# Performance work log

Measured on AMD Instinct MI355X. Metric: run time of the kernel, lower is better.

## Reference

```python
import jax, jax.numpy as jnp
import numpy as np

P = 2  # pooling_size

def setup_inputs() -> dict:
    key = jax.random.key(0)
    k1, k2, k3 = jax.random.split(key, 3)
    B, n, D = 16, 4096, 1024
    x = jax.random.normal(k1, (B, n, D), dtype=jnp.float32)
    W1 = jax.random.normal(k2, (D, D), dtype=jnp.float32) * (1.0 / np.sqrt(D))
    b1 = jnp.zeros((D,), dtype=jnp.float32)
    W2 = jax.random.normal(k3, (D, 1), dtype=jnp.float32) * (1.0 / np.sqrt(D))
    b2 = jnp.zeros((1,), dtype=jnp.float32)
    return {"x": x, "W1": W1, "b1": b1, "W2": W2, "b2": b2}

def reference(x, W1, b1, W2, b2):
    # x: [B, n, D] with n a perfect square; pool 2x2 windows via attention.
    B, n, D = x.shape
    s = int(n ** 0.5)
    g = s // P  # grid of regions per side
    # [B, g, P, g, P, D] -> [B, g, g, P, P, D] -> [B, R, P*P, D]
    # region order matches the original double loop (row-major over i, j).
    xg = (x.reshape(B, g, P, g, P, D)
            .transpose(0, 1, 3, 2, 4, 5)
            .reshape(B, g * g, P * P, D))
    # MLP scores (dropout is identity in eval mode)
    h = jax.nn.relu(jnp.einsum('brkd,de->brke', xg, W1) + b1)
    logits = jnp.einsum('brkd,d->brk', h, W2[:, 0]) + b2[0]
    alpha = jax.nn.softmax(logits, axis=-1)  # softmax over the P*P window
    # weighted sum over window -> [B, R, D]
    return jnp.einsum('brk,brkd->brd', alpha, xg)
```

## Files before the change

kernel.cpp:

```cpp
#include <hip/hip_runtime.h>
#include <hip/hip_bf16.h>

typedef float f32x4 __attribute__((ext_vector_type(4)));
typedef __bf16 bf16x8 __attribute__((ext_vector_type(8)));
typedef unsigned short ushort_t;
typedef ushort_t u16x8 __attribute__((ext_vector_type(8)));

#define GLDS16(gp, lp)                                                        \
  __builtin_amdgcn_global_load_lds(                                           \
      (__attribute__((address_space(1))) void*)(gp),                          \
      (__attribute__((address_space(3))) void*)(lp), 16, 0, 0)

__device__ __forceinline__ ushort_t f2bf(float f) {
  unsigned u = __float_as_uint(f);
  unsigned r = u + 0x7fffu + ((u >> 16) & 1u);
  return (ushort_t)(r >> 16);
}

__device__ __forceinline__ int swz(int row) {
  return (row & 3) ^ ((row >> 2) & 3);
}

__global__ __launch_bounds__(256) void prep_w1(const float* __restrict__ w1,
                                               ushort_t* __restrict__ w1t) {
  __shared__ ushort_t tile[64][80];
  const int k0 = blockIdx.x * 64;
  const int n0 = blockIdx.y * 64;
  const int tid = threadIdx.x;
#pragma unroll
  for (int it = 0; it < 16; ++it) {
    int idx = it * 256 + tid;
    int k = idx >> 6, n = idx & 63;
    tile[n][k] = f2bf(w1[(size_t)(k0 + k) * 1024 + n0 + n]);
  }
  __syncthreads();
#pragma unroll
  for (int it = 0; it < 2; ++it) {
    int idx = it * 256 + tid;
    int n = idx >> 3, kk = (idx & 7) * 8;
    bf16x8 v = *(const bf16x8*)&tile[n][kk];
    *(bf16x8*)&w1t[(size_t)(n0 + n) * 1024 + k0 + kk] = v;
  }
}

__global__ __launch_bounds__(256) void prep_x(const float* __restrict__ x,
                                              ushort_t* __restrict__ xbf) {
  size_t i = ((size_t)blockIdx.x * 256 + threadIdx.x) * 8;
  float4 a = *(const float4*)(x + i);
  float4 b = *(const float4*)(x + i + 4);
  u16x8 o;
  o[0] = f2bf(a.x); o[1] = f2bf(a.y); o[2] = f2bf(a.z); o[3] = f2bf(a.w);
  o[4] = f2bf(b.x); o[5] = f2bf(b.y); o[6] = f2bf(b.z); o[7] = f2bf(b.w);
  *(u16x8*)(xbf + i) = o;
}

#define FOLD_EPILOGUE(ACC)                                                    \
  {                                                                           \
    float bv[4], wv[4];                                                       \
    _Pragma("unroll") for (int ni = 0; ni < 4; ++ni) {                        \
      int col = nt * 256 + wn + ni * 16 + lc;                                 \
      bv[ni] = b1[col];                                                       \
      wv[ni] = w2[col];                                                       \
    }                                                                         \
    _Pragma("unroll") for (int mi = 0; mi < 4; ++mi)                          \
        _Pragma("unroll") for (int r = 0; r < 4; ++r) {                       \
      float s = 0.f;                                                          \
      _Pragma("unroll") for (int ni = 0; ni < 4; ++ni) {                      \
        float h = ACC[mi][ni][r] + bv[ni];                                    \
        h = h > 0.f ? h : 0.f;                                                \
        s += h * wv[ni];                                                      \
      }                                                                       \
      racc[mi][r] += s;                                                       \
    }                                                                         \
  }

template <bool A_BF16>
__global__ __launch_bounds__(512, 4) void gemm_fused(
    const void* __restrict__ aglob, const ushort_t* __restrict__ w1t,
    const float* __restrict__ b1, const float* __restrict__ w2,
    const float* __restrict__ x, float* __restrict__ out) {
  __shared__ ushort_t As[2][128 * 32];
  __shared__ ushort_t Bs[2][256 * 32];
  __shared__ float lbuf[128];
  __shared__ float abuf[128];

  const int tid = threadIdx.x;
  const int wave = tid >> 6, lane = tid & 63;
  const int quad = lane >> 4, lc = lane & 15;
  const int m0 = blockIdx.x * 128;
  const int wm = (wave & 1) * 64, wn = (wave >> 1) * 64;

  const int rA = tid >> 2, cA = (tid & 3) ^ swz(tid >> 2);
  const int rB0 = tid >> 2, cB0 = (tid & 3) ^ swz(rB0);
  const int rB1 = 128 + (tid >> 2), cB1 = (tid & 3) ^ swz(rB1);

  const ushort_t* abf = nullptr;
  const float* af = nullptr;
  if constexpr (A_BF16) {
    abf = (const ushort_t*)aglob + (size_t)(m0 + rA) * 1024 + cA * 8;
  } else {
    af = (const float*)aglob + (size_t)(m0 + rA) * 1024 + cA * 8;
  }
  const ushort_t* bp0 = w1t + (size_t)rB0 * 1024 + cB0 * 8;
  const ushort_t* bp1 = w1t + (size_t)rB1 * 1024 + cB1 * 8;

  int aoff[4], boff[4];
#pragma unroll
  for (int mi = 0; mi < 4; ++mi) {
    int r = wm + mi * 16 + lc;
    aoff[mi] = r * 32 + (quad ^ swz(r)) * 8;
  }
#pragma unroll
  for (int ni = 0; ni < 4; ++ni) {
    int r = wn + ni * 16 + lc;
    boff[ni] = r * 32 + (quad ^ swz(r)) * 8;
  }

  auto stage = [&](int buf, int nt_, int kt_) {
    const size_t cb = (size_t)nt_ * (256 * 1024);
    const int k0 = kt_ * 32;
    GLDS16(bp0 + cb + k0, &Bs[buf][tid * 8]);
    GLDS16(bp1 + cb + k0, &Bs[buf][(512 + tid) * 8]);
    if constexpr (A_BF16) {
      GLDS16(abf + k0, &As[buf][tid * 8]);
    } else {
      float4 v0 = *(const float4*)(af + k0);
      float4 v1 = *(const float4*)(af + k0 + 4);
      u16x8 o0;
      o0[0] = f2bf(v0.x); o0[1] = f2bf(v0.y); o0[2] = f2bf(v0.z); o0[3] = f2bf(v0.w);
      o0[4] = f2bf(v1.x); o0[5] = f2bf(v1.y); o0[6] = f2bf(v1.z); o0[7] = f2bf(v1.w);
      *(u16x8*)&As[buf][tid * 8] = o0;
    }
  };

  float racc[4][4] = {};

  stage(0, 0, 0);
  __syncthreads();

  for (int nt = 0; nt < 4; ++nt) {
    f32x4 acc[4][4] = {};
#pragma unroll 2
    for (int kt = 0; kt < 32; ++kt) {
      const int cur = kt & 1;
      if (!(nt == 3 && kt == 31)) {
        int nk = kt + 1, nn = nt;
        if (nk == 32) { nk = 0; nn = nt + 1; }
        stage(cur ^ 1, nn, nk);
      }

      bf16x8 afr[4], bfr[4];
#pragma unroll
      for (int mi = 0; mi < 4; ++mi) afr[mi] = *(const bf16x8*)&As[cur][aoff[mi]];
#pragma unroll
      for (int ni = 0; ni < 4; ++ni) bfr[ni] = *(const bf16x8*)&Bs[cur][boff[ni]];
#pragma unroll
      for (int mi = 0; mi < 4; ++mi)
#pragma unroll
        for (int ni = 0; ni < 4; ++ni)
          acc[mi][ni] = __builtin_amdgcn_mfma_f32_16x16x32_bf16(
              afr[mi], bfr[ni], acc[mi][ni], 0, 0, 0);
      __syncthreads();
    }
    FOLD_EPILOGUE(acc)
  }

#pragma unroll
  for (int mi = 0; mi < 4; ++mi)
#pragma unroll
    for (int r = 0; r < 4; ++r)
#pragma unroll
      for (int off = 1; off < 16; off <<= 1)
        racc[mi][r] += __shfl_xor(racc[mi][r], off, 64);
  __syncthreads();
  if (tid < 128) lbuf[tid] = 0.f;
  __syncthreads();
  if (lc == 0) {
#pragma unroll
    for (int mi = 0; mi < 4; ++mi)
#pragma unroll
      for (int r = 0; r < 4; ++r)
        atomicAdd(&lbuf[wm + mi * 16 + quad * 4 + r], racc[mi][r]);
  }
  __syncthreads();

  if (tid < 32) {
    const int j = tid;
    float l0 = lbuf[2 * j], l1 = lbuf[2 * j + 1];
    float l2 = lbuf[64 + 2 * j], l3 = lbuf[65 + 2 * j];
    float mx = fmaxf(fmaxf(l0, l1), fmaxf(l2, l3));
    float e0 = __expf(l0 - mx), e1 = __expf(l1 - mx);
    float e2 = __expf(l2 - mx), e3 = __expf(l3 - mx);
    float inv = 1.0f / (e0 + e1 + e2 + e3);
    abuf[j * 4 + 0] = e0 * inv;
    abuf[j * 4 + 1] = e1 * inv;
    abuf[j * 4 + 2] = e2 * inv;
    abuf[j * 4 + 3] = e3 * inv;
  }
  __syncthreads();

  const int b = blockIdx.x >> 5, ii = blockIdx.x & 31;
  const int jj = tid >> 8, t = tid & 255;
  const float* xs = x + (size_t)m0 * 1024;
  float* orow = out + ((size_t)(b * 1024 + ii * 32)) * 1024;
  for (int j0 = 0; j0 < 32; j0 += 2) {
    int j = j0 + jj;
    float a0 = abuf[j * 4 + 0], a1 = abuf[j * 4 + 1];
    float a2 = abuf[j * 4 + 2], a3 = abuf[j * 4 + 3];
    const float4* p0 = (const float4*)(xs + (size_t)(2 * j) * 1024);
    const float4* p1 = (const float4*)(xs + (size_t)(2 * j + 1) * 1024);
    const float4* p2 = (const float4*)(xs + (size_t)(64 + 2 * j) * 1024);
    const float4* p3 = (const float4*)(xs + (size_t)(65 + 2 * j) * 1024);
    float4 v0 = p0[t], v1 = p1[t], v2 = p2[t], v3 = p3[t];
    float4 o;
    o.x = a0 * v0.x + a1 * v1.x + a2 * v2.x + a3 * v3.x;
    o.y = a0 * v0.y + a1 * v1.y + a2 * v2.y + a3 * v3.y;
    o.z = a0 * v0.z + a1 * v1.z + a2 * v2.z + a3 * v3.z;
    o.w = a0 * v0.w + a1 * v1.w + a2 * v2.w + a3 * v3.w;
    ((float4*)(orow + (size_t)j * 1024))[t] = o;
  }
}

extern "C" void kernel_launch(void* const* d_in, const int* in_sizes, int n_in,
                              void* d_out, int out_size, void* d_ws,
                              size_t ws_size, hipStream_t stream) {
  const float* x  = (const float*)d_in[0];
  const float* W1 = (const float*)d_in[1];
  const float* b1 = (const float*)d_in[2];
  const float* W2 = (const float*)d_in[3];
  float* out = (float*)d_out;

  const size_t XBF_BYTES = 134217728ull;
  const size_t W1T_BYTES = 2097152ull;

  if (ws_size >= XBF_BYTES + W1T_BYTES) {
    ushort_t* xbf = (ushort_t*)d_ws;
    ushort_t* w1t = (ushort_t*)((char*)d_ws + XBF_BYTES);
    prep_x<<<32768, 256, 0, stream>>>(x, xbf);
    prep_w1<<<dim3(16, 16), 256, 0, stream>>>(W1, w1t);
    gemm_fused<true><<<512, 512, 0, stream>>>(xbf, w1t, b1, W2, x, out);
  } else {
    ushort_t* w1t = (ushort_t*)d_ws;
    prep_w1<<<dim3(16, 16), 256, 0, stream>>>(W1, w1t);
    gemm_fused<false><<<512, 512, 0, stream>>>(x, w1t, b1, W2, x, out);
  }
}
```

Measured before the change: 581.2 us.

## Enlarge GEMM tile to 256 rows with triple-buffered LDS pipeline

Doubles the per-block M tile from 128 to 256 rows, so each block reuses every W1 tile across twice as many rows and the grid halves to 256 blocks. The K loop becomes a flattened 128-step loop over a 3-stage LDS ring with raw s_barrier and explicit vmcnt waits, split into two MFMA halves with setprio so loads for step T+2 overlap compute. The cost is higher register and LDS use per block, lower occupancy (launch bounds 2), and only 256 blocks to cover the CUs, plus hand-written waitcnt logic that could be fragile.

```diff
diff --git a/kernel.cpp b/kernel.cpp
--- a/kernel.cpp
+++ b/kernel.cpp
@@ -10,6 +10,9 @@
   __builtin_amdgcn_global_load_lds(                                           \
       (__attribute__((address_space(1))) void*)(gp),                          \
       (__attribute__((address_space(3))) void*)(lp), 16, 0, 0)
+
+#define RAW_BARRIER() asm volatile("s_barrier" ::: "memory")
+#define WAIT_VMCNT(n) asm volatile("s_waitcnt vmcnt(" #n ")" ::: "memory")
 
 __device__ __forceinline__ ushort_t f2bf(float f) {
   unsigned u = __float_as_uint(f);
@@ -62,7 +65,7 @@
       bv[ni] = b1[col];                                                       \
       wv[ni] = w2[col];                                                       \
     }                                                                         \
-    _Pragma("unroll") for (int mi = 0; mi < 4; ++mi)                          \
+    _Pragma("unroll") for (int mi = 0; mi < 8; ++mi)                          \
         _Pragma("unroll") for (int r = 0; r < 4; ++r) {                       \
       float s = 0.f;                                                          \
       _Pragma("unroll") for (int ni = 0; ni < 4; ++ni) {                      \
@@ -75,38 +78,38 @@
   }
 
 template <bool A_BF16>
-__global__ __launch_bounds__(512, 4) void gemm_fused(
+__global__ __launch_bounds__(512, 2) void gemm_fused(
     const void* __restrict__ aglob, const ushort_t* __restrict__ w1t,
     const float* __restrict__ b1, const float* __restrict__ w2,
     const float* __restrict__ x, float* __restrict__ out) {
-  __shared__ ushort_t As[2][128 * 32];
-  __shared__ ushort_t Bs[2][256 * 32];
-  __shared__ float lbuf[128];
-  __shared__ float abuf[128];
+  __shared__ ushort_t As[3][256 * 32];
+  __shared__ ushort_t Bs[3][256 * 32];
+  __shared__ float lbuf[256];
+  __shared__ float abuf[256];
 
   const int tid = threadIdx.x;
   const int wave = tid >> 6, lane = tid & 63;
   const int quad = lane >> 4, lc = lane & 15;
-  const int m0 = blockIdx.x * 128;
-  const int wm = (wave & 1) * 64, wn = (wave >> 1) * 64;
+  const int m0 = blockIdx.x * 256;
+  const int wm = (wave & 1) * 128, wn = (wave >> 1) * 64;
 
   const int rA = tid >> 2, cA = (tid & 3) ^ swz(tid >> 2);
-  const int rB0 = tid >> 2, cB0 = (tid & 3) ^ swz(rB0);
-  const int rB1 = 128 + (tid >> 2), cB1 = (tid & 3) ^ swz(rB1);
-
-  const ushort_t* abf = nullptr;
-  const float* af = nullptr;
+
+  const ushort_t* abf0 = nullptr; const ushort_t* abf1 = nullptr;
+  const float* af0 = nullptr; const float* af1 = nullptr;
   if constexpr (A_BF16) {
-    abf = (const ushort_t*)aglob + (size_t)(m0 + rA) * 1024 + cA * 8;
+    abf0 = (const ushort_t*)aglob + (size_t)(m0 + rA) * 1024 + cA * 8;
+    abf1 = (const ushort_t*)aglob + (size_t)(m0 + 128 + rA) * 1024 + cA * 8;
   } else {
-    af = (const float*)aglob + (size_t)(m0 + rA) * 1024 + cA * 8;
-  }
-  const ushort_t* bp0 = w1t + (size_t)rB0 * 1024 + cB0 * 8;
-  const ushort_t* bp1 = w1t + (size_t)rB1 * 1024 + cB1 * 8;
-
-  int aoff[4], boff[4];
-#pragma unroll
-  for (int mi = 0; mi < 4; ++mi) {
+    af0 = (const float*)aglob + (size_t)(m0 + rA) * 1024 + cA * 8;
+    af1 = (const float*)aglob + (size_t)(m0 + 128 + rA) * 1024 + cA * 8;
+  }
+  const ushort_t* bq0 = w1t + (size_t)rA * 1024 + cA * 8;
+  const ushort_t* bq1 = w1t + (size_t)(128 + rA) * 1024 + cA * 8;
+
+  int aoff[8], boff[4];
+#pragma unroll
+  for (int mi = 0; mi < 8; ++mi) {
     int r = wm + mi * 16 + lc;
     aoff[mi] = r * 32 + (quad ^ swz(r)) * 8;
   }
@@ -116,108 +119,153 @@
     boff[ni] = r * 32 + (quad ^ swz(r)) * 8;
   }
 
-  auto stage = [&](int buf, int nt_, int kt_) {
-    const size_t cb = (size_t)nt_ * (256 * 1024);
-    const int k0 = kt_ * 32;
-    GLDS16(bp0 + cb + k0, &Bs[buf][tid * 8]);
-    GLDS16(bp1 + cb + k0, &Bs[buf][(512 + tid) * 8]);
+  auto stageA = [&](int buf, int T) {
+    const int k0 = (T & 31) * 32;
     if constexpr (A_BF16) {
-      GLDS16(abf + k0, &As[buf][tid * 8]);
+      GLDS16(abf0 + k0, &As[buf][tid * 8]);
+      GLDS16(abf1 + k0, &As[buf][(512 + tid) * 8]);
     } else {
-      float4 v0 = *(const float4*)(af + k0);
-      float4 v1 = *(const float4*)(af + k0 + 4);
-      u16x8 o0;
+      float4 v0 = *(const float4*)(af0 + k0);
+      float4 v1 = *(const float4*)(af0 + k0 + 4);
+      float4 v2 = *(const float4*)(af1 + k0);
+      float4 v3 = *(const float4*)(af1 + k0 + 4);
+      u16x8 o0, o1;
       o0[0] = f2bf(v0.x); o0[1] = f2bf(v0.y); o0[2] = f2bf(v0.z); o0[3] = f2bf(v0.w);
       o0[4] = f2bf(v1.x); o0[5] = f2bf(v1.y); o0[6] = f2bf(v1.z); o0[7] = f2bf(v1.w);
+      o1[0] = f2bf(v2.x); o1[1] = f2bf(v2.y); o1[2] = f2bf(v2.z); o1[3] = f2bf(v2.w);
+      o1[4] = f2bf(v3.x); o1[5] = f2bf(v3.y); o1[6] = f2bf(v3.z); o1[7] = f2bf(v3.w);
       *(u16x8*)&As[buf][tid * 8] = o0;
+      *(u16x8*)&As[buf][(512 + tid) * 8] = o1;
     }
   };
-
-  float racc[4][4] = {};
-
-  stage(0, 0, 0);
-  __syncthreads();
-
-  for (int nt = 0; nt < 4; ++nt) {
-    f32x4 acc[4][4] = {};
-#pragma unroll 2
-    for (int kt = 0; kt < 32; ++kt) {
-      const int cur = kt & 1;
-      if (!(nt == 3 && kt == 31)) {
-        int nk = kt + 1, nn = nt;
-        if (nk == 32) { nk = 0; nn = nt + 1; }
-        stage(cur ^ 1, nn, nk);
-      }
-
-      bf16x8 afr[4], bfr[4];
-#pragma unroll
-      for (int mi = 0; mi < 4; ++mi) afr[mi] = *(const bf16x8*)&As[cur][aoff[mi]];
-#pragma unroll
-      for (int ni = 0; ni < 4; ++ni) bfr[ni] = *(const bf16x8*)&Bs[cur][boff[ni]];
-#pragma unroll
-      for (int mi = 0; mi < 4; ++mi)
-#pragma unroll
-        for (int ni = 0; ni < 4; ++ni)
-          acc[mi][ni] = __builtin_amdgcn_mfma_f32_16x16x32_bf16(
-              afr[mi], bfr[ni], acc[mi][ni], 0, 0, 0);
-      __syncthreads();
+  auto stageB = [&](int buf, int T) {
+    const int k0 = (T & 31) * 32;
+    const size_t cb = (size_t)(T >> 5) * (256 * 1024);
+    GLDS16(bq0 + cb + k0, &Bs[buf][tid * 8]);
+    GLDS16(bq1 + cb + k0, &Bs[buf][(512 + tid) * 8]);
+  };
+
+  float racc[8][4] = {};
+  f32x4 acc[8][4] = {};
+
+  stageA(0, 0); stageB(0, 0);
+  stageA(1, 1); stageB(1, 1);
+  if constexpr (A_BF16) { WAIT_VMCNT(4); } else { WAIT_VMCNT(2);
+    asm volatile("s_waitcnt lgkmcnt(0)" ::: "memory"); }
+  RAW_BARRIER();
+
+  int cur = 0;
+#pragma unroll 1
+  for (int T = 0; T < 128; ++T) {
+    const int nt = T >> 5;
+    int stg = cur + 2; if (stg >= 3) stg -= 3;
+    const bool doStage = (T + 2 < 128);
+
+    if (doStage) stageA(stg, T + 2);
+    bf16x8 afr[4], bfr[4];
+#pragma unroll
+    for (int mi = 0; mi < 4; ++mi) afr[mi] = *(const bf16x8*)&As[cur][aoff[mi]];
+#pragma unroll
+    for (int ni = 0; ni < 4; ++ni) bfr[ni] = *(const bf16x8*)&Bs[cur][boff[ni]];
+    RAW_BARRIER();
+    __builtin_amdgcn_sched_barrier(0);
+    __builtin_amdgcn_s_setprio(1);
+#pragma unroll
+    for (int mi = 0; mi < 4; ++mi)
+#pragma unroll
+      for (int ni = 0; ni < 4; ++ni)
+        acc[mi][ni] = __builtin_amdgcn_mfma_f32_16x16x32_bf16(
+            afr[mi], bfr[ni], acc[mi][ni], 0, 0, 0);
+    __builtin_amdgcn_s_setprio(0);
+    RAW_BARRIER();
+
+    if (doStage) stageB(stg, T + 2);
+    bf16x8 afr2[4];
+#pragma unroll
+    for (int mi = 0; mi < 4; ++mi)
+      afr2[mi] = *(const bf16x8*)&As[cur][aoff[4 + mi]];
+    RAW_BARRIER();
+    __builtin_amdgcn_sched_barrier(0);
+    __builtin_amdgcn_s_setprio(1);
+#pragma unroll
+    for (int mi = 0; mi < 4; ++mi)
+#pragma unroll
+      for (int ni = 0; ni < 4; ++ni)
+        acc[4 + mi][ni] = __builtin_amdgcn_mfma_f32_16x16x32_bf16(
+            afr2[mi], bfr[ni], acc[4 + mi][ni], 0, 0, 0);
+    __builtin_amdgcn_s_setprio(0);
+
+    if constexpr (!A_BF16) asm volatile("s_waitcnt lgkmcnt(0)" ::: "memory");
+    if (T <= 125) { WAIT_VMCNT(4); } else { WAIT_VMCNT(0); }
+    RAW_BARRIER();
+    cur = cur + 1; if (cur >= 3) cur = 0;
+
+    if ((T & 31) == 31) {
+      FOLD_EPILOGUE(acc)
+#pragma unroll
+      for (int mi = 0; mi < 8; ++mi)
+#pragma unroll
+        for (int ni = 0; ni < 4; ++ni) acc[mi][ni] = (f32x4){0.f, 0.f, 0.f, 0.f};
     }
-    FOLD_EPILOGUE(acc)
-  }
-
-#pragma unroll
-  for (int mi = 0; mi < 4; ++mi)
+  }
+
+#pragma unroll
+  for (int mi = 0; mi < 8; ++mi)
 #pragma unroll
     for (int r = 0; r < 4; ++r)
 #pragma unroll
       for (int off = 1; off < 16; off <<= 1)
         racc[mi][r] += __shfl_xor(racc[mi][r], off, 64);
   __syncthreads();
-  if (tid < 128) lbuf[tid] = 0.f;
+  if (tid < 256) lbuf[tid] = 0.f;
   __syncthreads();
   if (lc == 0) {
 #pragma unroll
-    for (int mi = 0; mi < 4; ++mi)
+    for (int mi = 0; mi < 8; ++mi)
 #pragma unroll
       for (int r = 0; r < 4; ++r)
         atomicAdd(&lbuf[wm + mi * 16 + quad * 4 + r], racc[mi][r]);
   }
   __syncthreads();
 
-  if (tid < 32) {
-    const int j = tid;
-    float l0 = lbuf[2 * j], l1 = lbuf[2 * j + 1];
-    float l2 = lbuf[64 + 2 * j], l3 = lbuf[65 + 2 * j];
+  if (tid < 64) {
+    const int s = tid >> 5, j = tid & 31, base = s * 128;
+    float l0 = lbuf[base + 2 * j], l1 = lbuf[base + 2 * j + 1];
+    float l2 = lbuf[base + 64 + 2 * j], l3 = lbuf[base + 65 + 2 * j];
     float mx = fmaxf(fmaxf(l0, l1), fmaxf(l2, l3));
     float e0 = __expf(l0 - mx), e1 = __expf(l1 - mx);
     float e2 = __expf(l2 - mx), e3 = __expf(l3 - mx);
     float inv = 1.0f / (e0 + e1 + e2 + e3);
-    abuf[j * 4 + 0] = e0 * inv;
-    abuf[j * 4 + 1] = e1 * inv;
-    abuf[j * 4 + 2] = e2 * inv;
-    abuf[j * 4 + 3] = e3 * inv;
-  }
-  __syncthreads();
-
-  const int b = blockIdx.x >> 5, ii = blockIdx.x & 31;
+    abuf[tid * 4 + 0] = e0 * inv;
+    abuf[tid * 4 + 1] = e1 * inv;
+    abuf[tid * 4 + 2] = e2 * inv;
+    abuf[tid * 4 + 3] = e3 * inv;
+  }
+  __syncthreads();
+
   const int jj = tid >> 8, t = tid & 255;
-  const float* xs = x + (size_t)m0 * 1024;
-  float* orow = out + ((size_t)(b * 1024 + ii * 32)) * 1024;
-  for (int j0 = 0; j0 < 32; j0 += 2) {
-    int j = j0 + jj;
-    float a0 = abuf[j * 4 + 0], a1 = abuf[j * 4 + 1];
-    float a2 = abuf[j * 4 + 2], a3 = abuf[j * 4 + 3];
-    const float4* p0 = (const float4*)(xs + (size_t)(2 * j) * 1024);
-    const float4* p1 = (const float4*)(xs + (size_t)(2 * j + 1) * 1024);
-    const float4* p2 = (const float4*)(xs + (size_t)(64 + 2 * j) * 1024);
-    const float4* p3 = (const float4*)(xs + (size_t)(65 + 2 * j) * 1024);
-    float4 v0 = p0[t], v1 = p1[t], v2 = p2[t], v3 = p3[t];
-    float4 o;
-    o.x = a0 * v0.x + a1 * v1.x + a2 * v2.x + a3 * v3.x;
-    o.y = a0 * v0.y + a1 * v1.y + a2 * v2.y + a3 * v3.y;
-    o.z = a0 * v0.z + a1 * v1.z + a2 * v2.z + a3 * v3.z;
-    o.w = a0 * v0.w + a1 * v1.w + a2 * v2.w + a3 * v3.w;
-    ((float4*)(orow + (size_t)j * 1024))[t] = o;
+#pragma unroll 1
+  for (int s = 0; s < 2; ++s) {
+    const int g = blockIdx.x * 2 + s;
+    const int b = g >> 5, ii = g & 31;
+    const float* xs = x + (size_t)(m0 + s * 128) * 1024;
+    float* orow = out + ((size_t)(b * 1024 + ii * 32)) * 1024;
+    for (int j0 = 0; j0 < 32; j0 += 2) {
+      int j = j0 + jj;
+      float a0 = abuf[s * 128 + j * 4 + 0], a1 = abuf[s * 128 + j * 4 + 1];
+      float a2 = abuf[s * 128 + j * 4 + 2], a3 = abuf[s * 128 + j * 4 + 3];
+      const float4* p0 = (const float4*)(xs + (size_t)(2 * j) * 1024);
+      const float4* p1 = (const float4*)(xs + (size_t)(2 * j + 1) * 1024);
+      const float4* p2 = (const float4*)(xs + (size_t)(64 + 2 * j) * 1024);
+      const float4* p3 = (const float4*)(xs + (size_t)(65 + 2 * j) * 1024);
+      float4 v0 = p0[t], v1 = p1[t], v2 = p2[t], v3 = p3[t];
+      float4 o;
+      o.x = a0 * v0.x + a1 * v1.x + a2 * v2.x + a3 * v3.x;
+      o.y = a0 * v0.y + a1 * v1.y + a2 * v2.y + a3 * v3.y;
+      o.z = a0 * v0.z + a1 * v1.z + a2 * v2.z + a3 * v3.z;
+      o.w = a0 * v0.w + a1 * v1.w + a2 * v2.w + a3 * v3.w;
+      ((float4*)(orow + (size_t)j * 1024))[t] = o;
+    }
   }
 }
 
@@ -238,10 +286,10 @@
     ushort_t* w1t = (ushort_t*)((char*)d_ws + XBF_BYTES);
     prep_x<<<32768, 256, 0, stream>>>(x, xbf);
     prep_w1<<<dim3(16, 16), 256, 0, stream>>>(W1, w1t);
-    gemm_fused<true><<<512, 512, 0, stream>>>(xbf, w1t, b1, W2, x, out);
+    gemm_fused<true><<<256, 512, 0, stream>>>(xbf, w1t, b1, W2, x, out);
   } else {
     ushort_t* w1t = (ushort_t*)d_ws;
     prep_w1<<<dim3(16, 16), 256, 0, stream>>>(W1, w1t);
-    gemm_fused<false><<<512, 512, 0, stream>>>(x, w1t, b1, W2, x, out);
-  }
-}
+    gemm_fused<false><<<256, 512, 0, stream>>>(x, w1t, b1, W2, x, out);
+  }
+}
```

New measurement: 609.2 us. 1.05x slower.

## Triple-buffer GEMM LDS staging with vmcnt waits and grid-stride prep_x

Applied to the files above, without the earlier changes.

The fused GEMM moves from a double-buffered K loop with a full __syncthreads each step to a flattened 128-step loop over a three-slot LDS ring. Each step prefetches two stages ahead and uses explicit s_waitcnt vmcnt plus a raw s_barrier, so global-to-LDS loads overlap more compute and each barrier waits only for the oldest stage. The bf16 conversion kernel becomes grid-stride with 2048 blocks instead of 32768. The extra LDS buffer may lower occupancy, and the hand-written waitcnt counts must match the loads actually issued or results will be wrong.

```diff
diff --git a/kernel.cpp b/kernel.cpp
--- a/kernel.cpp
+++ b/kernel.cpp
@@ -10,6 +10,9 @@
   __builtin_amdgcn_global_load_lds(                                           \
       (__attribute__((address_space(1))) void*)(gp),                          \
       (__attribute__((address_space(3))) void*)(lp), 16, 0, 0)
+
+#define RAW_BARRIER() asm volatile("s_barrier" ::: "memory")
+#define WAIT_VMCNT(n) asm volatile("s_waitcnt vmcnt(" #n ")" ::: "memory")
 
 __device__ __forceinline__ ushort_t f2bf(float f) {
   unsigned u = __float_as_uint(f);
@@ -45,13 +48,18 @@
 
 __global__ __launch_bounds__(256) void prep_x(const float* __restrict__ x,
                                               ushort_t* __restrict__ xbf) {
-  size_t i = ((size_t)blockIdx.x * 256 + threadIdx.x) * 8;
-  float4 a = *(const float4*)(x + i);
-  float4 b = *(const float4*)(x + i + 4);
-  u16x8 o;
-  o[0] = f2bf(a.x); o[1] = f2bf(a.y); o[2] = f2bf(a.z); o[3] = f2bf(a.w);
-  o[4] = f2bf(b.x); o[5] = f2bf(b.y); o[6] = f2bf(b.z); o[7] = f2bf(b.w);
-  *(u16x8*)(xbf + i) = o;
+  const size_t nchunks = 8388608ull;
+  const size_t stride = (size_t)gridDim.x * 256;
+  for (size_t c = (size_t)blockIdx.x * 256 + threadIdx.x; c < nchunks;
+       c += stride) {
+    size_t i = c * 8;
+    float4 a = *(const float4*)(x + i);
+    float4 b = *(const float4*)(x + i + 4);
+    u16x8 o;
+    o[0] = f2bf(a.x); o[1] = f2bf(a.y); o[2] = f2bf(a.z); o[3] = f2bf(a.w);
+    o[4] = f2bf(b.x); o[5] = f2bf(b.y); o[6] = f2bf(b.z); o[7] = f2bf(b.w);
+    *(u16x8*)(xbf + i) = o;
+  }
 }
 
 #define FOLD_EPILOGUE(ACC)                                                    \
@@ -79,8 +87,8 @@
     const void* __restrict__ aglob, const ushort_t* __restrict__ w1t,
     const float* __restrict__ b1, const float* __restrict__ w2,
     const float* __restrict__ x, float* __restrict__ out) {
-  __shared__ ushort_t As[2][128 * 32];
-  __shared__ ushort_t Bs[2][256 * 32];
+  __shared__ ushort_t As[3 * 128 * 32];
+  __shared__ ushort_t Bs[3 * 256 * 32];
   __shared__ float lbuf[128];
   __shared__ float abuf[128];
 
@@ -116,53 +124,72 @@
     boff[ni] = r * 32 + (quad ^ swz(r)) * 8;
   }
 
-  auto stage = [&](int buf, int nt_, int kt_) {
+  auto stage = [&](int buf, int T_) {
+    const int nt_ = T_ >> 5, kt_ = T_ & 31;
     const size_t cb = (size_t)nt_ * (256 * 1024);
     const int k0 = kt_ * 32;
-    GLDS16(bp0 + cb + k0, &Bs[buf][tid * 8]);
-    GLDS16(bp1 + cb + k0, &Bs[buf][(512 + tid) * 8]);
+    ushort_t* Bsb = Bs + buf * 8192;
+    ushort_t* Asb = As + buf * 4096;
+    GLDS16(bp0 + cb + k0, Bsb + tid * 8);
+    GLDS16(bp1 + cb + k0, Bsb + (512 + tid) * 8);
     if constexpr (A_BF16) {
-      GLDS16(abf + k0, &As[buf][tid * 8]);
+      GLDS16(abf + k0, Asb + tid * 8);
     } else {
       float4 v0 = *(const float4*)(af + k0);
       float4 v1 = *(const float4*)(af + k0 + 4);
-      u16x8 o0;
-      o0[0] = f2bf(v0.x); o0[1] = f2bf(v0.y); o0[2] = f2bf(v0.z); o0[3] = f2bf(v0.w);
-      o0[4] = f2bf(v1.x); o0[5] = f2bf(v1.y); o0[6] = f2bf(v1.z); o0[7] = f2bf(v1.w);
-      *(u16x8*)&As[buf][tid * 8] = o0;
+      u16x8 o;
+      o[0] = f2bf(v0.x); o[1] = f2bf(v0.y); o[2] = f2bf(v0.z); o[3] = f2bf(v0.w);
+      o[4] = f2bf(v1.x); o[5] = f2bf(v1.y); o[6] = f2bf(v1.z); o[7] = f2bf(v1.w);
+      *(u16x8*)(Asb + tid * 8) = o;
     }
   };
 
   float racc[4][4] = {};
-
-  stage(0, 0, 0);
-  __syncthreads();
-
-  for (int nt = 0; nt < 4; ++nt) {
-    f32x4 acc[4][4] = {};
-#pragma unroll 2
-    for (int kt = 0; kt < 32; ++kt) {
-      const int cur = kt & 1;
-      if (!(nt == 3 && kt == 31)) {
-        int nk = kt + 1, nn = nt;
-        if (nk == 32) { nk = 0; nn = nt + 1; }
-        stage(cur ^ 1, nn, nk);
-      }
-
-      bf16x8 afr[4], bfr[4];
-#pragma unroll
-      for (int mi = 0; mi < 4; ++mi) afr[mi] = *(const bf16x8*)&As[cur][aoff[mi]];
-#pragma unroll
-      for (int ni = 0; ni < 4; ++ni) bfr[ni] = *(const bf16x8*)&Bs[cur][boff[ni]];
+  f32x4 acc[4][4] = {};
+
+  stage(0, 0);
+  stage(1, 1);
+  if constexpr (A_BF16) { WAIT_VMCNT(3); }
+  else { WAIT_VMCNT(2); asm volatile("s_waitcnt lgkmcnt(0)" ::: "memory"); }
+  RAW_BARRIER();
+
+  int bc = 0;
+#pragma unroll 1
+  for (int T = 0; T < 128; ++T) {
+    const int nt = T >> 5;
+    int sb = bc + 2; if (sb >= 3) sb -= 3;
+    if (T < 126) stage(sb, T + 2);
+
+    const ushort_t* Asc = As + bc * 4096;
+    const ushort_t* Bsc = Bs + bc * 8192;
+    bf16x8 afr[4], bfr[4];
+#pragma unroll
+    for (int mi = 0; mi < 4; ++mi) afr[mi] = *(const bf16x8*)&Asc[aoff[mi]];
+#pragma unroll
+    for (int ni = 0; ni < 4; ++ni) bfr[ni] = *(const bf16x8*)&Bsc[boff[ni]];
+#pragma unroll
+    for (int mi = 0; mi < 4; ++mi)
+#pragma unroll
+      for (int ni = 0; ni < 4; ++ni)
+        acc[mi][ni] = __builtin_amdgcn_mfma_f32_16x16x32_bf16(
+            afr[mi], bfr[ni], acc[mi][ni], 0, 0, 0);
+
+    if ((T & 31) == 31) {
+      FOLD_EPILOGUE(acc)
 #pragma unroll
       for (int mi = 0; mi < 4; ++mi)
 #pragma unroll
-        for (int ni = 0; ni < 4; ++ni)
-          acc[mi][ni] = __builtin_amdgcn_mfma_f32_16x16x32_bf16(
-              afr[mi], bfr[ni], acc[mi][ni], 0, 0, 0);
-      __syncthreads();
+        for (int ni = 0; ni < 4; ++ni) acc[mi][ni] = (f32x4){0.f, 0.f, 0.f, 0.f};
     }
-    FOLD_EPILOGUE(acc)
+
+    if constexpr (A_BF16) {
+      if (T < 126) { WAIT_VMCNT(3); }
+      else if (T == 126) { WAIT_VMCNT(0); }
+    } else {
+      asm volatile("s_waitcnt vmcnt(0) lgkmcnt(0)" ::: "memory");
+    }
+    if (T < 127) RAW_BARRIER();
+    bc = (bc == 2) ? 0 : bc + 1;
   }
 
 #pragma unroll
@@ -236,7 +263,7 @@
   if (ws_size >= XBF_BYTES + W1T_BYTES) {
     ushort_t* xbf = (ushort_t*)d_ws;
     ushort_t* w1t = (ushort_t*)((char*)d_ws + XBF_BYTES);
-    prep_x<<<32768, 256, 0, stream>>>(x, xbf);
+    prep_x<<<2048, 256, 0, stream>>>(x, xbf);
     prep_w1<<<dim3(16, 16), 256, 0, stream>>>(W1, w1t);
     gemm_fused<true><<<512, 512, 0, stream>>>(xbf, w1t, b1, W2, x, out);
   } else {
```

New measurement: 592.3 us. About the same (+1.9%).
